# Kernel tuning notes

Measured on AMD Instinct MI355X. Metric: run time of the kernel, lower is better.

## Reference

```python
import jax, jax.numpy as jnp
import numpy as np

N_NODES = 1000000
N_EDGES = 32000000
NUM_GRAPHS = 1024


def setup_inputs() -> dict:
    key = jax.random.key(0)
    k1, k2, k3, k4, k5 = jax.random.split(key, 5)
    x = jax.random.normal(k1, (N_NODES, 1), dtype=jnp.float32)
    W = jax.random.normal(k2, (1, 1), dtype=jnp.float32)
    b = jax.random.normal(k3, (1,), dtype=jnp.float32)
    edge_index = jax.random.randint(k4, (2, N_EDGES), 0, N_NODES, dtype=jnp.int64)
    batch = jnp.sort(jax.random.randint(k5, (N_NODES,), 0, NUM_GRAPHS, dtype=jnp.int64))
    return {"x": x, "W": W, "b": b, "edge_index": edge_index, "batch": batch}


def reference(x, W, b, edge_index, batch):
    src, dst = edge_index[0], edge_index[1]
    # SimpleConv (default sum aggregation): out[i] = sum_{(j->i) in E} x[j]
    agg = jax.ops.segment_sum(x[src], dst, num_segments=N_NODES)  # [N,1]
    h = jax.nn.relu(agg)
    # global_mean_pool over graph ids
    sums = jax.ops.segment_sum(h, batch, num_segments=NUM_GRAPHS)  # [G,1]
    counts = jax.ops.segment_sum(jnp.ones((N_NODES,), dtype=h.dtype), batch,
                                 num_segments=NUM_GRAPHS)  # [G]
    pooled = sums / jnp.maximum(counts, 1.0)[:, None]
    # Linear(1 -> 1): y = pooled @ W^T + b
    return pooled @ W.T + b
```

## Files before the change

### kernel.cpp

```cpp
#include <hip/hip_runtime.h>

#define N_NODES    1000000
#define N_EDGES    32000000
#define NUM_GRAPHS 1024

typedef int          vint4  __attribute__((ext_vector_type(4)));
typedef unsigned int uint32;
typedef unsigned int vuint2 __attribute__((ext_vector_type(2)));
typedef unsigned int vuint4 __attribute__((ext_vector_type(4)));

#define BUCKET_SHIFT 12
#define BUCKET_NODES (1 << BUCKET_SHIFT)
#define NBUCKETS     245

#define T1_NCHUNK   512
#define T1_BLOCK    512
#define T1_EDGES_PER_CHUNK (N_EDGES / T1_NCHUNK)
#define T1_QUADS    (T1_EDGES_PER_CHUNK / 4)
#define T1_ROUNDS   ((T1_QUADS + T1_BLOCK - 1) / T1_BLOCK)
#define SCAP        64
#define SLAB_CAP    352
#define RSPLIT      2
#define CELLS_HALF  (T1_NCHUNK / RSPLIT)

#define T2_CAP      136192
#define T2_NCHUNK   512
#define T2_EPC      (N_EDGES / T2_NCHUNK)

__global__ __launch_bounds__(T1_BLOCK)
void slab_scatter(const int* __restrict__ src,
                  const int* __restrict__ dst,
                  uint32* __restrict__ slab,
                  vuint2* __restrict__ cnt_g) {
    __shared__ uint32 stage[NBUCKETS][SCAP];
    __shared__ uint32 rpos[NBUCKETS];
    __shared__ uint32 ecnt[NBUCKETS];
    __shared__ uint32 flushed[NBUCKETS];
    __shared__ uint32 carry[NBUCKETS];

    const int tid = threadIdx.x;
    const int w   = blockIdx.x;
    const vint4* d4 = (const vint4*)(dst + (size_t)w * T1_EDGES_PER_CHUNK);
    const vint4* s4 = (const vint4*)(src + (size_t)w * T1_EDGES_PER_CHUNK);

    for (int b = tid; b < NBUCKETS; b += T1_BLOCK) {
        rpos[b] = 0; ecnt[b] = 0; flushed[b] = 0; carry[b] = 0;
    }
    __syncthreads();

    const int grp    = tid >> 4;
    const int lane16 = tid & 15;

    for (int r = 0; r < T1_ROUNDS; ++r) {
        int q = r * T1_BLOCK + tid;
        if (q < T1_QUADS) {
            vint4 d = d4[q];
            vint4 s = s4[q];
            #pragma unroll
            for (int k = 0; k < 4; ++k) {
                uint32 dd = (uint32)(k == 0 ? d.x : k == 1 ? d.y : k == 2 ? d.z : d.w);
                uint32 ss = (uint32)(k == 0 ? s.x : k == 1 ? s.y : k == 2 ? s.z : s.w);
                uint32 b  = dd >> BUCKET_SHIFT;
                uint32 v  = ((dd & (BUCKET_NODES - 1)) << 20) | ss;
                uint32 c  = carry[b] + atomicAdd(&rpos[b], 1u);
                if (c < SCAP) {
                    stage[b][c] = v;
                } else {
                    uint32 e = atomicAdd(&ecnt[b], 1u);
                    slab[((size_t)b * T1_NCHUNK + w) * SLAB_CAP + (SLAB_CAP - 1 - e)] = v;
                }
            }
        }
        __syncthreads();
        for (int b = grp; b < NBUCKETS; b += 32) {
            uint32 tot = carry[b] + rpos[b];
            if (tot > SCAP) tot = SCAP;
            uint32 lines = tot >> 4;
            uint32 rem   = tot & 15u;
            uint32 fl    = flushed[b];
            uint32* dp = slab + ((size_t)b * T1_NCHUNK + w) * SLAB_CAP + fl;
            for (uint32 l = 0; l < lines; ++l)
                __builtin_nontemporal_store(stage[b][l * 16 + lane16], &dp[l * 16 + lane16]);
            if (lines) {
                uint32 mv = 0;
                if (lane16 < rem) mv = stage[b][lines * 16 + lane16];
                if (lane16 < rem) stage[b][lane16] = mv;
            }
            if (lane16 == 0) {
                flushed[b] = fl + lines * 16;
                carry[b]   = rem;
                rpos[b]    = 0;
            }
        }
        __syncthreads();
    }
    for (int b = grp; b < NBUCKETS; b += 32) {
        uint32 rem = carry[b];
        uint32 fl  = flushed[b];
        uint32* dp = slab + ((size_t)b * T1_NCHUNK + w) * SLAB_CAP + fl;
        if (lane16 < rem)
            __builtin_nontemporal_store(stage[b][lane16], &dp[lane16]);
        if (lane16 == 0) {
            vuint2 c; c.x = fl + rem; c.y = ecnt[b];
            cnt_g[(size_t)b * T1_NCHUNK + w] = c;
        }
    }
}

__global__ __launch_bounds__(1024)
void slab_reduce_split(const uint32* __restrict__ slab,
                       const vuint2* __restrict__ cnt_g,
                       const float* __restrict__ x,
                       float* __restrict__ pacc) {
    __shared__ float acc[BUCKET_NODES];
    const int blk = blockIdx.x;
    const int b   = blk >> 1;
    const int h   = blk & 1;
    const int tid = threadIdx.x;
    for (int n = tid; n < BUCKET_NODES; n += 1024) acc[n] = 0.0f;
    __syncthreads();

    const int wv = tid >> 6, lane = tid & 63;
    const size_t cbase = (size_t)b * T1_NCHUNK + h * CELLS_HALF + wv * 16;

    vuint2 mc; mc.x = 0; mc.y = 0;
    if (lane < 16) mc = cnt_g[cbase + lane];

    for (int j = 0; j < 16; j += 2) {
        uint32 f0 = __shfl(mc.x, j),     e0 = __shfl(mc.y, j);
        uint32 f1 = __shfl(mc.x, j + 1), e1 = __shfl(mc.y, j + 1);
        const uint32* c0 = slab + (cbase + j) * SLAB_CAP;
        const uint32* c1 = slab + (cbase + j + 1) * SLAB_CAP;
        const vuint4* p0 = (const vuint4*)c0;
        const vuint4* p1 = (const vuint4*)c1;
        uint32 n0 = f0 >> 2, n1 = f1 >> 2;
        uint32 nmax = n0 > n1 ? n0 : n1;
        for (uint32 i = lane; i < nmax; i += 64) {
            bool a = i < n0, c = i < n1;
            vuint4 va, vc;
            if (a) va = __builtin_nontemporal_load(&p0[i]);
            if (c) vc = __builtin_nontemporal_load(&p1[i]);
            float xa0, xa1, xa2, xa3, xc0, xc1, xc2, xc3;
            if (a) { xa0 = x[va.x & 0xFFFFFu]; xa1 = x[va.y & 0xFFFFFu];
                     xa2 = x[va.z & 0xFFFFFu]; xa3 = x[va.w & 0xFFFFFu]; }
            if (c) { xc0 = x[vc.x & 0xFFFFFu]; xc1 = x[vc.y & 0xFFFFFu];
                     xc2 = x[vc.z & 0xFFFFFu]; xc3 = x[vc.w & 0xFFFFFu]; }
            if (a) {
                atomicAdd(&acc[va.x >> 20], xa0);
                atomicAdd(&acc[va.y >> 20], xa1);
                atomicAdd(&acc[va.z >> 20], xa2);
                atomicAdd(&acc[va.w >> 20], xa3);
            }
            if (c) {
                atomicAdd(&acc[vc.x >> 20], xc0);
                atomicAdd(&acc[vc.y >> 20], xc1);
                atomicAdd(&acc[vc.z >> 20], xc2);
                atomicAdd(&acc[vc.w >> 20], xc3);
            }
        }
        for (uint32 i = (n0 << 2) + lane; i < f0; i += 64) {
            uint32 v = c0[i];
            atomicAdd(&acc[v >> 20], x[v & 0xFFFFFu]);
        }
        for (uint32 i = (n1 << 2) + lane; i < f1; i += 64) {
            uint32 v = c1[i];
            atomicAdd(&acc[v >> 20], x[v & 0xFFFFFu]);
        }
        for (uint32 i = lane; i < e0; i += 64) {
            uint32 v = c0[SLAB_CAP - 1 - i];
            atomicAdd(&acc[v >> 20], x[v & 0xFFFFFu]);
        }
        for (uint32 i = lane; i < e1; i += 64) {
            uint32 v = c1[SLAB_CAP - 1 - i];
            atomicAdd(&acc[v >> 20], x[v & 0xFFFFFu]);
        }
    }
    __syncthreads();

    float* dp = pacc + (size_t)blk * BUCKET_NODES;
    for (int n = tid; n < BUCKET_NODES; n += 1024)
        dp[n] = acc[n];
}

__global__ __launch_bounds__(1024)
void merge_pool(const float* __restrict__ pacc,
                const int* __restrict__ batch,
                float* __restrict__ sums,
                float* __restrict__ counts) {
    const int b = blockIdx.x;
    const int tid = threadIdx.x;
    const float* p0 = pacc + (size_t)(2 * b) * BUCKET_NODES;
    const float* p1 = p0 + BUCKET_NODES;
    const int node0 = b << BUCKET_SHIFT;
    for (int n = tid; n < BUCKET_NODES; n += 1024) {
        int i = node0 + n;
        float h = 0.0f;
        int g = -1;
        if (i < N_NODES) {
            h = fmaxf(p0[n] + p1[n], 0.0f);
            g = batch[i];
        }
        int g0 = __shfl(g, 0);
        if (__all(g == g0)) {
            #pragma unroll
            for (int off = 32; off > 0; off >>= 1)
                h += __shfl_down(h, off);
            if ((tid & 63) == 0 && g0 >= 0) {
                atomicAdd(&sums[g0], h);
                atomicAdd(&counts[g0], 64.0f);
            }
        } else if (g >= 0) {
            atomicAdd(&sums[g], h);
            atomicAdd(&counts[g], 1.0f);
        }
    }
}

__global__ void finalize_kernel(const float* __restrict__ sums,
                                const float* __restrict__ counts,
                                const float* __restrict__ W,
                                const float* __restrict__ b,
                                float* __restrict__ out) {
    int g = blockIdx.x * blockDim.x + threadIdx.x;
    if (g < NUM_GRAPHS) {
        float pooled = sums[g] / fmaxf(counts[g], 1.0f);
        out[g] = pooled * W[0] + b[0];
    }
}

__global__ __launch_bounds__(1024)
void bucket_scatter(const int* __restrict__ src,
                    const int* __restrict__ dst,
                    uint32* __restrict__ sorted,
                    uint32* __restrict__ gpos) {
    __shared__ uint32 hist[NBUCKETS];
    __shared__ uint32 pos[NBUCKETS];
    const int tid = threadIdx.x;
    const size_t base = (size_t)blockIdx.x * T2_EPC;
    for (int b = tid; b < NBUCKETS; b += 1024) hist[b] = 0;
    __syncthreads();
    const vint4* d4 = (const vint4*)(dst + base);
    const vint4* s4 = (const vint4*)(src + base);
    const int nvec = T2_EPC / 4;
    for (int i = tid; i < nvec; i += 1024) {
        vint4 d = d4[i];
        atomicAdd(&hist[(uint32)d.x >> BUCKET_SHIFT], 1u);
        atomicAdd(&hist[(uint32)d.y >> BUCKET_SHIFT], 1u);
        atomicAdd(&hist[(uint32)d.z >> BUCKET_SHIFT], 1u);
        atomicAdd(&hist[(uint32)d.w >> BUCKET_SHIFT], 1u);
    }
    __syncthreads();
    for (int b = tid; b < NBUCKETS; b += 1024)
        pos[b] = atomicAdd(&gpos[b], hist[b]);
    __syncthreads();
    for (int i = tid; i < nvec; i += 1024) {
        vint4 d = d4[i];
        vint4 s = s4[i];
        #pragma unroll
        for (int k = 0; k < 4; ++k) {
            uint32 dd = (uint32)(k == 0 ? d.x : k == 1 ? d.y : k == 2 ? d.z : d.w);
            uint32 ss = (uint32)(k == 0 ? s.x : k == 1 ? s.y : k == 2 ? s.z : s.w);
            uint32 b = dd >> BUCKET_SHIFT, dl = dd & (BUCKET_NODES - 1);
            uint32 slot = atomicAdd(&pos[b], 1u);
            if (slot < T2_CAP) sorted[(size_t)b * T2_CAP + slot] = (dl << 20) | ss;
        }
    }
}

__global__ __launch_bounds__(1024)
void bucket_reduce(const uint32* __restrict__ sorted,
                   const uint32* __restrict__ gpos,
                   const float* __restrict__ x,
                   const int* __restrict__ batch,
                   float* __restrict__ sums,
                   float* __restrict__ counts) {
    __shared__ float acc[BUCKET_NODES];
    const int b = blockIdx.x;
    const int tid = threadIdx.x;
    for (int n = tid; n < BUCKET_NODES; n += 1024) acc[n] = 0.0f;
    __syncthreads();
    uint32 cnt = gpos[b];
    if (cnt > T2_CAP) cnt = T2_CAP;
    const uint32* reg = sorted + (size_t)b * T2_CAP;
    const vuint4* r4 = (const vuint4*)reg;
    const uint32 nvec = cnt / 4;
    for (uint32 i = tid; i < nvec; i += 1024) {
        vuint4 v = r4[i];
        atomicAdd(&acc[v.x >> 20], x[v.x & 0xFFFFFu]);
        atomicAdd(&acc[v.y >> 20], x[v.y & 0xFFFFFu]);
        atomicAdd(&acc[v.z >> 20], x[v.z & 0xFFFFFu]);
        atomicAdd(&acc[v.w >> 20], x[v.w & 0xFFFFFu]);
    }
    for (uint32 i = nvec * 4 + tid; i < cnt; i += 1024) {
        uint32 v = reg[i];
        atomicAdd(&acc[v >> 20], x[v & 0xFFFFFu]);
    }
    __syncthreads();
    const int node0 = b << BUCKET_SHIFT;
    for (int n = tid; n < BUCKET_NODES; n += 1024) {
        int i = node0 + n;
        float h = 0.0f;
        int g = -1;
        if (i < N_NODES) {
            h = fmaxf(acc[n], 0.0f);
            g = batch[i];
        }
        int g0 = __shfl(g, 0);
        if (__all(g == g0)) {
            #pragma unroll
            for (int off = 32; off > 0; off >>= 1)
                h += __shfl_down(h, off);
            if ((tid & 63) == 0 && g0 >= 0) {
                atomicAdd(&sums[g0], h);
                atomicAdd(&counts[g0], 64.0f);
            }
        } else if (g >= 0) {
            atomicAdd(&sums[g], h);
            atomicAdd(&counts[g], 1.0f);
        }
    }
}

__global__ void scatter_edges_dev(const vint4* __restrict__ src4,
                                  const vint4* __restrict__ dst4,
                                  const float* __restrict__ x,
                                  float* __restrict__ agg) {
    int t = blockIdx.x * blockDim.x + threadIdx.x;
    if (t < N_EDGES / 4) {
        vint4 s = __builtin_nontemporal_load(&src4[t]);
        vint4 d = __builtin_nontemporal_load(&dst4[t]);
        atomicAdd(&agg[d.x], x[s.x]);
        atomicAdd(&agg[d.y], x[s.y]);
        atomicAdd(&agg[d.z], x[s.z]);
        atomicAdd(&agg[d.w], x[s.w]);
    }
}

__global__ void pool_nodes_kernel(const float* __restrict__ agg,
                                  const int* __restrict__ batch,
                                  float* __restrict__ sums,
                                  float* __restrict__ counts) {
    int i = blockIdx.x * blockDim.x + threadIdx.x;
    float h = 0.0f;
    int g = -1;
    if (i < N_NODES) {
        h = fmaxf(agg[i], 0.0f);
        g = batch[i];
    }
    int g0 = __shfl(g, 0);
    if (__all(g == g0)) {
        #pragma unroll
        for (int off = 32; off > 0; off >>= 1)
            h += __shfl_down(h, off);
        if ((threadIdx.x & 63) == 0 && g0 >= 0) {
            atomicAdd(&sums[g0], h);
            atomicAdd(&counts[g0], 64.0f);
        }
    } else if (g >= 0) {
        atomicAdd(&sums[g], h);
        atomicAdd(&counts[g], 1.0f);
    }
}

extern "C" void kernel_launch(void* const* d_in, const int* in_sizes, int n_in,
                              void* d_out, int out_size, void* d_ws, size_t ws_size,
                              hipStream_t stream) {
    const float* x     = (const float*)d_in[0];
    const float* W     = (const float*)d_in[1];
    const float* b     = (const float*)d_in[2];
    const int*   edge  = (const int*)d_in[3];
    const int*   batch = (const int*)d_in[4];
    float* out = (float*)d_out;

    const int* src = edge;
    const int* dst = edge + N_EDGES;

    const size_t ncells     = (size_t)NBUCKETS * T1_NCHUNK;
    const size_t slab_elems = ncells * SLAB_CAP;
    const size_t pacc_elems = (size_t)NBUCKETS * RSPLIT * BUCKET_NODES;
    const size_t need1 = (slab_elems + 2 * ncells + pacc_elems + 2 * NUM_GRAPHS) * 4;
    const size_t t2_elems = (size_t)NBUCKETS * T2_CAP;
    const size_t need2 = (t2_elems + 256 + 2 * NUM_GRAPHS) * 4;

    if (ws_size >= need1) {
        uint32* slab   = (uint32*)d_ws;
        vuint2* cnt_g  = (vuint2*)(slab + slab_elems);
        float*  pacc   = (float*)(slab + slab_elems + 2 * ncells);
        float*  sums   = pacc + pacc_elems;
        float*  counts = sums + NUM_GRAPHS;
        (void)hipMemsetAsync(sums, 0, 2 * NUM_GRAPHS * 4, stream);

        slab_scatter<<<T1_NCHUNK, T1_BLOCK, 0, stream>>>(src, dst, slab, cnt_g);
        slab_reduce_split<<<NBUCKETS * RSPLIT, 1024, 0, stream>>>(slab, cnt_g, x, pacc);
        merge_pool<<<NBUCKETS, 1024, 0, stream>>>(pacc, batch, sums, counts);
        finalize_kernel<<<(NUM_GRAPHS + 255) / 256, 256, 0, stream>>>(sums, counts, W, b, out);
    } else if (ws_size >= need2) {
        uint32* sorted = (uint32*)d_ws;
        uint32* gpos   = sorted + t2_elems;
        float*  sums   = (float*)(gpos + 256);
        float*  counts = sums + NUM_GRAPHS;
        (void)hipMemsetAsync(gpos, 0, (256 + 2 * NUM_GRAPHS) * 4, stream);

        bucket_scatter<<<T2_NCHUNK, 1024, 0, stream>>>(src, dst, sorted, gpos);
        bucket_reduce<<<NBUCKETS, 1024, 0, stream>>>(sorted, gpos, x, batch, sums, counts);
        finalize_kernel<<<(NUM_GRAPHS + 255) / 256, 256, 0, stream>>>(sums, counts, W, b, out);
    } else {
        float* agg    = (float*)d_ws;
        float* sums   = agg + N_NODES;
        float* counts = sums + NUM_GRAPHS;
        (void)hipMemsetAsync(d_ws, 0, ((size_t)N_NODES + 2 * NUM_GRAPHS) * 4, stream);

        int nthreads = N_EDGES / 4;
        scatter_edges_dev<<<(nthreads + 255) / 256, 256, 0, stream>>>(
            (const vint4*)src, (const vint4*)dst, x, agg);
        pool_nodes_kernel<<<(N_NODES + 255) / 256, 256, 0, stream>>>(agg, batch, sums, counts);
        finalize_kernel<<<(NUM_GRAPHS + 255) / 256, 256, 0, stream>>>(sums, counts, W, b, out);
    }
}
```

Measured before the change: 632.1 us.

## Split bucket reduction four ways with smaller blocks and four-cell interleaving

The reduction now splits each bucket across four blocks of 512 threads instead of two blocks of 1024, and each wave processes four slab cells at once instead of two, issuing more independent gathers per iteration. The merge kernel sums four partial accumulators instead of two, and the slab capacity per cell shrinks slightly. This aims to raise memory-level parallelism and block-scheduling granularity in the gather-heavy reduction. In exchange it writes and reads twice as many partial accumulator arrays, drops the nontemporal load hints, and uses more registers per thread. The smaller slab capacity also risks overflow if a cell ever holds more entries.

```diff
diff --git a/kernel.cpp b/kernel.cpp
--- a/kernel.cpp
+++ b/kernel.cpp
@@ -19,9 +19,10 @@
 #define T1_QUADS    (T1_EDGES_PER_CHUNK / 4)
 #define T1_ROUNDS   ((T1_QUADS + T1_BLOCK - 1) / T1_BLOCK)
 #define SCAP        64
-#define SLAB_CAP    352
-#define RSPLIT      2
-#define CELLS_HALF  (T1_NCHUNK / RSPLIT)
+#define SLAB_CAP    336
+#define RSPLIT      4
+#define CELLS_PART  (T1_NCHUNK / RSPLIT)
+#define RBLOCK      512
 
 #define T2_CAP      136192
 #define T2_NCHUNK   512
@@ -107,78 +108,77 @@
     }
 }
 
-__global__ __launch_bounds__(1024)
+__global__ __launch_bounds__(RBLOCK)
 void slab_reduce_split(const uint32* __restrict__ slab,
                        const vuint2* __restrict__ cnt_g,
                        const float* __restrict__ x,
                        float* __restrict__ pacc) {
     __shared__ float acc[BUCKET_NODES];
     const int blk = blockIdx.x;
-    const int b   = blk >> 1;
-    const int h   = blk & 1;
+    const int b   = blk >> 2;
+    const int h   = blk & 3;
     const int tid = threadIdx.x;
-    for (int n = tid; n < BUCKET_NODES; n += 1024) acc[n] = 0.0f;
+    for (int n = tid; n < BUCKET_NODES; n += RBLOCK) acc[n] = 0.0f;
     __syncthreads();
 
     const int wv = tid >> 6, lane = tid & 63;
-    const size_t cbase = (size_t)b * T1_NCHUNK + h * CELLS_HALF + wv * 16;
+    const size_t cbase = (size_t)b * T1_NCHUNK + h * CELLS_PART + wv * 16;
 
     vuint2 mc; mc.x = 0; mc.y = 0;
     if (lane < 16) mc = cnt_g[cbase + lane];
 
-    for (int j = 0; j < 16; j += 2) {
-        uint32 f0 = __shfl(mc.x, j),     e0 = __shfl(mc.y, j);
-        uint32 f1 = __shfl(mc.x, j + 1), e1 = __shfl(mc.y, j + 1);
-        const uint32* c0 = slab + (cbase + j) * SLAB_CAP;
-        const uint32* c1 = slab + (cbase + j + 1) * SLAB_CAP;
-        const vuint4* p0 = (const vuint4*)c0;
-        const vuint4* p1 = (const vuint4*)c1;
-        uint32 n0 = f0 >> 2, n1 = f1 >> 2;
-        uint32 nmax = n0 > n1 ? n0 : n1;
+    for (int j = 0; j < 16; j += 4) {
+        uint32 f[4], e[4], nq[4];
+        const uint32* cp[4];
+        uint32 nmax = 0;
+        #pragma unroll
+        for (int k = 0; k < 4; ++k) {
+            f[k]  = __shfl(mc.x, j + k);
+            e[k]  = __shfl(mc.y, j + k);
+            cp[k] = slab + (cbase + j + k) * SLAB_CAP;
+            nq[k] = f[k] >> 2;
+            nmax  = nq[k] > nmax ? nq[k] : nmax;
+        }
         for (uint32 i = lane; i < nmax; i += 64) {
-            bool a = i < n0, c = i < n1;
-            vuint4 va, vc;
-            if (a) va = __builtin_nontemporal_load(&p0[i]);
-            if (c) vc = __builtin_nontemporal_load(&p1[i]);
-            float xa0, xa1, xa2, xa3, xc0, xc1, xc2, xc3;
-            if (a) { xa0 = x[va.x & 0xFFFFFu]; xa1 = x[va.y & 0xFFFFFu];
-                     xa2 = x[va.z & 0xFFFFFu]; xa3 = x[va.w & 0xFFFFFu]; }
-            if (c) { xc0 = x[vc.x & 0xFFFFFu]; xc1 = x[vc.y & 0xFFFFFu];
-                     xc2 = x[vc.z & 0xFFFFFu]; xc3 = x[vc.w & 0xFFFFFu]; }
-            if (a) {
-                atomicAdd(&acc[va.x >> 20], xa0);
-                atomicAdd(&acc[va.y >> 20], xa1);
-                atomicAdd(&acc[va.z >> 20], xa2);
-                atomicAdd(&acc[va.w >> 20], xa3);
-            }
-            if (c) {
-                atomicAdd(&acc[vc.x >> 20], xc0);
-                atomicAdd(&acc[vc.y >> 20], xc1);
-                atomicAdd(&acc[vc.z >> 20], xc2);
-                atomicAdd(&acc[vc.w >> 20], xc3);
-            }
-        }
-        for (uint32 i = (n0 << 2) + lane; i < f0; i += 64) {
-            uint32 v = c0[i];
-            atomicAdd(&acc[v >> 20], x[v & 0xFFFFFu]);
-        }
-        for (uint32 i = (n1 << 2) + lane; i < f1; i += 64) {
-            uint32 v = c1[i];
-            atomicAdd(&acc[v >> 20], x[v & 0xFFFFFu]);
-        }
-        for (uint32 i = lane; i < e0; i += 64) {
-            uint32 v = c0[SLAB_CAP - 1 - i];
-            atomicAdd(&acc[v >> 20], x[v & 0xFFFFFu]);
-        }
-        for (uint32 i = lane; i < e1; i += 64) {
-            uint32 v = c1[SLAB_CAP - 1 - i];
-            atomicAdd(&acc[v >> 20], x[v & 0xFFFFFu]);
+            bool  m[4];
+            vuint4 v[4];
+            #pragma unroll
+            for (int k = 0; k < 4; ++k) {
+                m[k] = i < nq[k];
+                if (m[k]) v[k] = ((const vuint4*)cp[k])[i];
+            }
+            float xs[4][4];
+            #pragma unroll
+            for (int k = 0; k < 4; ++k) if (m[k]) {
+                xs[k][0] = x[v[k].x & 0xFFFFFu];
+                xs[k][1] = x[v[k].y & 0xFFFFFu];
+                xs[k][2] = x[v[k].z & 0xFFFFFu];
+                xs[k][3] = x[v[k].w & 0xFFFFFu];
+            }
+            #pragma unroll
+            for (int k = 0; k < 4; ++k) if (m[k]) {
+                atomicAdd(&acc[v[k].x >> 20], xs[k][0]);
+                atomicAdd(&acc[v[k].y >> 20], xs[k][1]);
+                atomicAdd(&acc[v[k].z >> 20], xs[k][2]);
+                atomicAdd(&acc[v[k].w >> 20], xs[k][3]);
+            }
+        }
+        #pragma unroll
+        for (int k = 0; k < 4; ++k) {
+            for (uint32 i = (nq[k] << 2) + lane; i < f[k]; i += 64) {
+                uint32 v = cp[k][i];
+                atomicAdd(&acc[v >> 20], x[v & 0xFFFFFu]);
+            }
+            for (uint32 i = lane; i < e[k]; i += 64) {
+                uint32 v = cp[k][SLAB_CAP - 1 - i];
+                atomicAdd(&acc[v >> 20], x[v & 0xFFFFFu]);
+            }
         }
     }
     __syncthreads();
 
     float* dp = pacc + (size_t)blk * BUCKET_NODES;
-    for (int n = tid; n < BUCKET_NODES; n += 1024)
+    for (int n = tid; n < BUCKET_NODES; n += RBLOCK)
         dp[n] = acc[n];
 }
 
@@ -189,15 +189,16 @@
                 float* __restrict__ counts) {
     const int b = blockIdx.x;
     const int tid = threadIdx.x;
-    const float* p0 = pacc + (size_t)(2 * b) * BUCKET_NODES;
-    const float* p1 = p0 + BUCKET_NODES;
+    const float* p0 = pacc + (size_t)(RSPLIT * b) * BUCKET_NODES;
     const int node0 = b << BUCKET_SHIFT;
     for (int n = tid; n < BUCKET_NODES; n += 1024) {
         int i = node0 + n;
         float h = 0.0f;
         int g = -1;
         if (i < N_NODES) {
-            h = fmaxf(p0[n] + p1[n], 0.0f);
+            float a = p0[n] + p0[BUCKET_NODES + n]
+                    + p0[2 * BUCKET_NODES + n] + p0[3 * BUCKET_NODES + n];
+            h = fmaxf(a, 0.0f);
             g = batch[i];
         }
         int g0 = __shfl(g, 0);
@@ -391,7 +392,7 @@
         (void)hipMemsetAsync(sums, 0, 2 * NUM_GRAPHS * 4, stream);
 
         slab_scatter<<<T1_NCHUNK, T1_BLOCK, 0, stream>>>(src, dst, slab, cnt_g);
-        slab_reduce_split<<<NBUCKETS * RSPLIT, 1024, 0, stream>>>(slab, cnt_g, x, pacc);
+        slab_reduce_split<<<NBUCKETS * RSPLIT, RBLOCK, 0, stream>>>(slab, cnt_g, x, pacc);
         merge_pool<<<NBUCKETS, 1024, 0, stream>>>(pacc, batch, sums, counts);
         finalize_kernel<<<(NUM_GRAPHS + 255) / 256, 256, 0, stream>>>(sums, counts, W, b, out);
     } else if (ws_size >= need2) {
```

New measurement: 644.8 us. +2.0%, slower.
